# Optimization experiments

Measured on AMD Instinct MI355X. Metric: run time of the kernel, lower is better.

The kernel has to match this reference:

```python
import jax, jax.numpy as jnp
import numpy as np

B, LQ, LK, D = 16, 2048, 2048, 64
EPS = 1e-13
KEEP_PROB = 0.8  # fraction of key positions kept in the mask


def setup_inputs() -> dict:
    key = jax.random.key(0)
    kq, kk, kv, km = jax.random.split(key, 4)
    q = jax.random.normal(kq, (B, LQ, D), dtype=jnp.float32)
    k = jax.random.normal(kk, (B, LK, D), dtype=jnp.float32)
    v = jax.random.normal(kv, (B, LK, D), dtype=jnp.float32)
    # binary 0/1 float mask over key positions (ESIM-style padding mask)
    v_mask = (jax.random.uniform(km, (B, LK)) < KEEP_PROB).astype(jnp.float32)
    return {"q": q, "k": k, "v": v, "v_mask": v_mask}


def masked_softmax(scores, mask):
    # ESIM masked_softmax: softmax(scores * mask) * mask, renormalized.
    m = mask[:, None, :]  # [B, 1, Lk] broadcast over query dim
    p = jax.nn.softmax(scores * m, axis=-1) * m
    return p / (jnp.sum(p, axis=-1, keepdims=True) + EPS)


def reference(q, k, v, v_mask):
    scores = jnp.einsum("bqd,bkd->bqk", q, k)  # [B, Lq, Lk]
    attend = masked_softmax(scores, v_mask)
    return jnp.einsum("bqk,bkd->bqd", attend, v)  # [B, Lq, D]
```

## Files before the change

### kernel.cpp

```cpp
#include <hip/hip_runtime.h>
#include <hip/hip_bf16.h>
#include <stdint.h>

#define NB 16
#define SLQ 2048
#define SLK 2048
#define DD 64
#define BQ 64
#define BK 64
#define NT (SLK / BK)
#define QTILES (SLQ / BQ)
#define LOG2E 1.44269504f

typedef _Float16 f16x8 __attribute__((ext_vector_type(8)));
typedef short s16x8 __attribute__((ext_vector_type(8)));
typedef unsigned int u32x4 __attribute__((ext_vector_type(4)));
typedef unsigned short u16x4 __attribute__((ext_vector_type(4)));
typedef float f32x4 __attribute__((ext_vector_type(4)));
typedef float f32x2 __attribute__((ext_vector_type(2)));

typedef __attribute__((address_space(1))) const void gvoid;
typedef __attribute__((address_space(3))) void lvoid;

__device__ __forceinline__ int swzb(int row, int bytecol) {
    return row * 128 + (bytecol ^ ((row & 7) << 4));
}

__device__ __forceinline__ void gload16(const void* g, void* l) {
    __builtin_amdgcn_global_load_lds((gvoid*)g, (lvoid*)l, 16, 0, 0);
}

__device__ __forceinline__ uint16_t f2bf(float f) {
    __bf16 h = (__bf16)f;
    return __builtin_bit_cast(uint16_t, h);
}
__device__ __forceinline__ float bf2f(uint16_t u) {
    uint32_t x = ((uint32_t)u) << 16;
    return __builtin_bit_cast(float, x);
}

__device__ __forceinline__ int pi64(int x) {
    return (x & 0x23) | ((x & 4) << 2) | ((x >> 1) & 0x0C);
}

__global__ __launch_bounds__(256)
void prep_all(const float* __restrict__ q, const float* __restrict__ k,
              const float* __restrict__ v, const float* __restrict__ vm,
              char* __restrict__ qs, char* __restrict__ ks,
              char* __restrict__ vts, uint16_t* __restrict__ mb16) {
    const int bid = blockIdx.x;
    if (bid < 1024) {
        const int tl = bid & 511;
        const bool isq = bid < 512;
        const float sc = isq ? LOG2E : 1.0f;
        const float* src = (isq ? q : k) + (size_t)tl * (BK * DD);
        char* dst = (isq ? qs : ks) + (size_t)tl * (BK * DD * 2);
        #pragma unroll
        for (int it = 0; it < 2; ++it) {
            int c = threadIdx.x + it * 256;
            int row = c >> 3, col8 = c & 7;
            f32x4 a  = *(const f32x4*)(src + row * DD + col8 * 8);
            f32x4 b2 = *(const f32x4*)(src + row * DD + col8 * 8 + 4);
            f16x8 h;
            #pragma unroll
            for (int j = 0; j < 4; ++j) {
                h[j] = (_Float16)(a[j] * sc);
                h[4 + j] = (_Float16)(b2[j] * sc);
            }
            *(f16x8*)(dst + swzb(row, col8 * 16)) = h;
        }
    } else if (bid < 1536) {
        const int tl = bid - 1024;
        const float* src = v + (size_t)tl * (BK * DD);
        const float* msk = vm + (size_t)tl * BK;
        char* dst = vts + (size_t)tl * (BK * DD * 2);
        const int d = threadIdx.x & 63;
        #pragma unroll
        for (int it = 0; it < 2; ++it) {
            int key8 = (threadIdx.x >> 6) + it * 4;
            s16x8 h;
            #pragma unroll
            for (int j = 0; j < 8; ++j) {
                int kp = key8 * 8 + j;
                int sk = pi64(kp);
                float mv = msk[sk];
                h[j] = (short)f2bf((mv != 0.f) ? src[sk * DD + d] : 0.f);
            }
            *(s16x8*)(dst + swzb(d, key8 * 16)) = h;
        }
    } else {
        int i = (bid - 1536) * 1024 + threadIdx.x * 4;
        int srci = (i & ~63) | pi64(i & 63);
        f32x4 m = *(const f32x4*)(vm + srci);
        u16x4 o;
        #pragma unroll
        for (int j = 0; j < 4; ++j) o[j] = (m[j] != 0.f) ? (uint16_t)0x3F80 : (uint16_t)0;
        *(u16x4*)(mb16 + i) = o;
    }
}

__global__ __launch_bounds__(256, 4)
void attn_fwd(const char* __restrict__ qs, const char* __restrict__ ks,
              const char* __restrict__ vts, const uint16_t* __restrict__ mb16,
              uint16_t* __restrict__ po, float* __restrict__ pl,
              float* __restrict__ out, int nsp)
{
    __shared__ __align__(16) char lk[2][BK * DD * 2];
    __shared__ __align__(16) char lv[2][BK * DD * 2];

    const int tid  = threadIdx.x;
    const int lane = tid & 63;
    const int w    = tid >> 6;
    const int lg   = lane >> 4;
    const int lm   = lane & 15;

    const int G = 512 * nsp;
    int wg = blockIdx.x;
    wg = (wg & 7) * (G >> 3) + (wg >> 3);
    const int qt   = wg & 31;
    const int rest = wg >> 5;
    const int sp   = rest % nsp;
    const int b    = rest / nsp;

    const int qq = NT / nsp, rm = NT % nsp;
    const int t0  = sp * qq + (sp < rm ? sp : rm);
    const int cnt = qq + (sp < rm ? 1 : 0);

    const char* qtile = qs  + (size_t)(b * 32 + qt) * 8192;
    const char* kbase = ks  + (size_t)(b * 32 + t0) * 8192;
    const char* vbase = vts + (size_t)(b * 32 + t0) * 8192;
    const uint16_t* mk = mb16 + (size_t)b * SLK + t0 * BK;

    #pragma unroll
    for (int i = 0; i < 2; ++i) {
        int ch = w * 2 + i;
        gload16(qtile + ch * 1024 + lane * 16, lk[1] + ch * 1024);
    }
    #pragma unroll
    for (int i = 0; i < 2; ++i) {
        int ch = w * 2 + i;
        gload16(kbase + ch * 1024 + lane * 16, lk[0] + ch * 1024);
        gload16(vbase + ch * 1024 + lane * 16, lv[0] + ch * 1024);
    }
    asm volatile("s_waitcnt vmcnt(0)" ::: "memory");
    __syncthreads();

    f16x8 qf[2];
    #pragma unroll
    for (int kc = 0; kc < 2; ++kc)
        qf[kc] = *(const f16x8*)(lk[1] + swzb(w * 16 + lm, kc * 64 + lg * 16));
    asm volatile("s_waitcnt lgkmcnt(0)" ::: "memory");
    __syncthreads();

    f32x4 oacc[4], rsacc;
    #pragma unroll
    for (int d = 0; d < 4; ++d) oacc[d] = (f32x4){0.f, 0.f, 0.f, 0.f};
    rsacc = (f32x4){0.f, 0.f, 0.f, 0.f};

    int buf = 0;
    for (int kt = 0; kt < cnt; ++kt) {
        s16x8 mf0 = *(const s16x8*)(mk + kt * BK + lg * 8);
        s16x8 mf1 = *(const s16x8*)(mk + kt * BK + 32 + lg * 8);

        if (kt + 1 < cnt) {
            const char* kg = kbase + (size_t)(kt + 1) * 8192;
            const char* vg = vbase + (size_t)(kt + 1) * 8192;
            #pragma unroll
            for (int i = 0; i < 2; ++i) {
                int ch = w * 2 + i;
                gload16(kg + ch * 1024 + lane * 16, lk[buf ^ 1] + ch * 1024);
                gload16(vg + ch * 1024 + lane * 16, lv[buf ^ 1] + ch * 1024);
            }
        }

        f32x4 s[4];
        #pragma unroll
        for (int f = 0; f < 4; ++f) s[f] = (f32x4){0.f, 0.f, 0.f, 0.f};
        #pragma unroll
        for (int f = 0; f < 4; ++f) {
            #pragma unroll
            for (int kc = 0; kc < 2; ++kc) {
                f16x8 kf = *(const f16x8*)(lk[buf] + swzb(f * 16 + lm, kc * 64 + lg * 16));
                s[f] = __builtin_amdgcn_mfma_f32_16x16x32_f16(kf, qf[kc], s[f], 0, 0, 0);
            }
        }

        uint32_t pw[8];
        #pragma unroll
        for (int f = 0; f < 4; ++f) {
            float p0 = __builtin_amdgcn_exp2f(s[f][0]);
            float p1 = __builtin_amdgcn_exp2f(s[f][1]);
            float p2 = __builtin_amdgcn_exp2f(s[f][2]);
            float p3 = __builtin_amdgcn_exp2f(s[f][3]);
            pw[f * 2]     = (uint32_t)f2bf(p0) | ((uint32_t)f2bf(p1) << 16);
            pw[f * 2 + 1] = (uint32_t)f2bf(p2) | ((uint32_t)f2bf(p3) << 16);
        }
        u32x4 wa = {pw[0], pw[1], pw[2], pw[3]};
        u32x4 wb = {pw[4], pw[5], pw[6], pw[7]};
        s16x8 pa0 = __builtin_bit_cast(s16x8, wa);
        s16x8 pa1 = __builtin_bit_cast(s16x8, wb);

        rsacc = __builtin_amdgcn_mfma_f32_16x16x32_bf16(pa0, mf0, rsacc, 0, 0, 0);
        rsacc = __builtin_amdgcn_mfma_f32_16x16x32_bf16(pa1, mf1, rsacc, 0, 0, 0);

        #pragma unroll
        for (int d = 0; d < 4; ++d) {
            s16x8 vf0 = *(const s16x8*)(lv[buf] + swzb(d * 16 + lm, lg * 16));
            s16x8 vf1 = *(const s16x8*)(lv[buf] + swzb(d * 16 + lm, 64 + lg * 16));
            oacc[d] = __builtin_amdgcn_mfma_f32_16x16x32_bf16(pa0, vf0, oacc[d], 0, 0, 0);
            oacc[d] = __builtin_amdgcn_mfma_f32_16x16x32_bf16(pa1, vf1, oacc[d], 0, 0, 0);
        }

        asm volatile("s_waitcnt vmcnt(0)" ::: "memory");
        __syncthreads();
        buf ^= 1;
    }

    if (nsp == 1) {
        float* ob = out + ((size_t)b * SLQ + (size_t)qt * BQ) * DD;
        #pragma unroll
        for (int i = 0; i < 4; ++i) {
            float inv = 1.f / (rsacc[i] + 1e-13f);
            int row = w * 16 + lg * 4 + i;
            #pragma unroll
            for (int d = 0; d < 4; ++d)
                ob[row * DD + d * 16 + lm] = oacc[d][i] * inv;
        }
    } else {
        uint16_t* pob = po + (size_t)wg * (BQ * DD);
        #pragma unroll
        for (int i = 0; i < 4; ++i) {
            int row = w * 16 + lg * 4 + i;
            #pragma unroll
            for (int d = 0; d < 4; ++d)
                pob[row * DD + d * 16 + lm] = f2bf(oacc[d][i]);
            if (lm == 0) pl[(size_t)wg * BQ + row] = rsacc[i];
        }
    }
}

__global__ __launch_bounds__(256)
void merge_k(const uint16_t* __restrict__ po, const float* __restrict__ pl,
             float* __restrict__ out, int nsp) {
    const int t  = blockIdx.x;
    const int b  = t >> 5, qt = t & 31;
    const int i0 = (b * nsp) * 32 + qt;
    const int r0 = threadIdx.x >> 4;
    const int c4 = (threadIdx.x & 15) * 4;
    float* ob = out + ((size_t)b * SLQ + (size_t)qt * BQ) * DD;
    #pragma unroll
    for (int rr = 0; rr < BQ; rr += 16) {
        int r = r0 + rr;
        float l = 1e-13f;
        f32x4 acc = (f32x4){0.f, 0.f, 0.f, 0.f};
        for (int s = 0; s < nsp; ++s) {
            int idx = i0 + s * 32;
            l += pl[(size_t)idx * BQ + r];
            u16x4 a = *(const u16x4*)(po + (size_t)idx * (BQ * DD) + r * DD + c4);
            #pragma unroll
            for (int j = 0; j < 4; ++j) acc[j] += bf2f(a[j]);
        }
        float inv = 1.f / l;
        f32x4 o;
        #pragma unroll
        for (int j = 0; j < 4; ++j) o[j] = acc[j] * inv;
        *(f32x4*)(ob + r * DD + c4) = o;
    }
}

__global__ __launch_bounds__(256, 2)
void attn_fallback(const float* __restrict__ q, const float* __restrict__ k,
                   const float* __restrict__ v, const float* __restrict__ vm,
                   float* __restrict__ out)
{
    __shared__ __align__(16) char lqh[64 * DD * 2];
    __shared__ __align__(16) char lql[64 * DD * 2];
    __shared__ __align__(16) char lkh[BK * DD * 2];
    __shared__ __align__(16) char lkl[BK * DD * 2];
    __shared__ __align__(16) char lvt[DD * BK * 2];
    __shared__ __align__(16) char lpp[64 * BK * 2];
    __shared__ float lmask[BK];

    const int tid  = threadIdx.x;
    const int lane = tid & 63;
    const int w    = tid >> 6;
    const int lg   = lane >> 4;
    const int lm   = lane & 15;

    const int b  = blockIdx.y;
    const int qt = blockIdx.x;

    const float* qb = q + ((size_t)b * SLQ + (size_t)qt * 64) * DD;
    const float* kb = k + (size_t)b * SLK * DD;
    const float* vb = v + (size_t)b * SLK * DD;
    const float* mb = vm + (size_t)b * SLK;

    #pragma unroll
    for (int it = 0; it < 2; ++it) {
        int c = tid + it * 256;
        int row = c >> 3, col8 = c & 7;
        f32x4 a  = *(const f32x4*)(qb + row * DD + col8 * 8);
        f32x4 bb = *(const f32x4*)(qb + row * DD + col8 * 8 + 4);
        s16x8 h, l;
        #pragma unroll
        for (int j = 0; j < 4; ++j) {
            uint16_t hh = f2bf(a[j]);
            h[j] = (short)hh; l[j] = (short)f2bf(a[j] - bf2f(hh));
            uint16_t hb = f2bf(bb[j]);
            h[4 + j] = (short)hb; l[4 + j] = (short)f2bf(bb[j] - bf2f(hb));
        }
        *(s16x8*)(lqh + swzb(row, col8 * 16)) = h;
        *(s16x8*)(lql + swzb(row, col8 * 16)) = l;
    }
    __syncthreads();

    s16x8 qfh[2], qfl[2];
    #pragma unroll
    for (int kc = 0; kc < 2; ++kc) {
        qfh[kc] = *(const s16x8*)(lqh + swzb(w * 16 + lm, kc * 64 + lg * 16));
        qfl[kc] = *(const s16x8*)(lql + swzb(w * 16 + lm, kc * 64 + lg * 16));
    }

    float mrow[4], lrow[4];
    f32x4 oacc[4];
    #pragma unroll
    for (int i = 0; i < 4; ++i) { mrow[i] = -1e30f; lrow[i] = 0.f; }
    #pragma unroll
    for (int d = 0; d < 4; ++d) oacc[d] = (f32x4){0.f, 0.f, 0.f, 0.f};

    for (int kt = 0; kt < NT; ++kt) {
        __syncthreads();
        const float* ks2 = kb + (size_t)kt * BK * DD;
        const float* vs = vb + (size_t)kt * BK * DD;

        #pragma unroll
        for (int it = 0; it < 2; ++it) {
            int c = tid + it * 256;
            int row = c >> 3, col8 = c & 7;
            f32x4 a  = *(const f32x4*)(ks2 + row * DD + col8 * 8);
            f32x4 bb = *(const f32x4*)(ks2 + row * DD + col8 * 8 + 4);
            s16x8 h, l;
            #pragma unroll
            for (int j = 0; j < 4; ++j) {
                uint16_t hh = f2bf(a[j]);
                h[j] = (short)hh; l[j] = (short)f2bf(a[j] - bf2f(hh));
                uint16_t hb = f2bf(bb[j]);
                h[4 + j] = (short)hb; l[4 + j] = (short)f2bf(bb[j] - bf2f(hb));
            }
            *(s16x8*)(lkh + swzb(row, col8 * 16)) = h;
            *(s16x8*)(lkl + swzb(row, col8 * 16)) = l;
        }
        #pragma unroll
        for (int it = 0; it < 8; ++it) {
            int c = tid + it * 256;
            int key = c >> 5, dp = (c & 31) * 2;
            f32x2 a = *(const f32x2*)(vs + key * DD + dp);
            *(uint16_t*)(lvt + swzb(dp,     key * 2)) = f2bf(a[0]);
            *(uint16_t*)(lvt + swzb(dp + 1, key * 2)) = f2bf(a[1]);
        }
        if (tid < BK) lmask[tid] = mb[kt * BK + tid];
        __syncthreads();

        f32x4 s[4];
        #pragma unroll
        for (int f = 0; f < 4; ++f) s[f] = (f32x4){0.f, 0.f, 0.f, 0.f};
        #pragma unroll
        for (int f = 0; f < 4; ++f) {
            #pragma unroll
            for (int kc = 0; kc < 2; ++kc) {
                s16x8 kfh = *(const s16x8*)(lkh + swzb(f * 16 + lm, kc * 64 + lg * 16));
                s16x8 kfl = *(const s16x8*)(lkl + swzb(f * 16 + lm, kc * 64 + lg * 16));
                s[f] = __builtin_amdgcn_mfma_f32_16x16x32_bf16(qfh[kc], kfh, s[f], 0, 0, 0);
                s[f] = __builtin_amdgcn_mfma_f32_16x16x32_bf16(qfh[kc], kfl, s[f], 0, 0, 0);
                s[f] = __builtin_amdgcn_mfma_f32_16x16x32_bf16(qfl[kc], kfh, s[f], 0, 0, 0);
            }
        }

        float mv[4];
        #pragma unroll
        for (int f = 0; f < 4; ++f) mv[f] = lmask[f * 16 + lm];

        float pmax[4];
        #pragma unroll
        for (int i = 0; i < 4; ++i) {
            float x = -1e30f;
            #pragma unroll
            for (int f = 0; f < 4; ++f) {
                float sv = (mv[f] != 0.f) ? s[f][i] : -1e30f;
                s[f][i] = sv;
                x = fmaxf(x, sv);
            }
            #pragma unroll
            for (int off = 1; off < 16; off <<= 1)
                x = fmaxf(x, __shfl_xor(x, off, 64));
            pmax[i] = x;
        }

        float scl[4];
        #pragma unroll
        for (int i = 0; i < 4; ++i) {
            float mn = fmaxf(mrow[i], pmax[i]);
            scl[i] = __expf(mrow[i] - mn);
            mrow[i] = mn;
        }
        float rs[4] = {0.f, 0.f, 0.f, 0.f};
        #pragma unroll
        for (int f = 0; f < 4; ++f) {
            #pragma unroll
            for (int i = 0; i < 4; ++i) {
                float p = __expf(s[f][i] - mrow[i]);
                s[f][i] = p;
                rs[i] += p;
            }
        }
        #pragma unroll
        for (int i = 0; i < 4; ++i) {
            #pragma unroll
            for (int off = 1; off < 16; off <<= 1)
                rs[i] += __shfl_xor(rs[i], off, 64);
            lrow[i] = lrow[i] * scl[i] + rs[i];
        }
        #pragma unroll
        for (int d = 0; d < 4; ++d)
            #pragma unroll
            for (int i = 0; i < 4; ++i)
                oacc[d][i] *= scl[i];

        #pragma unroll
        for (int f = 0; f < 4; ++f)
            #pragma unroll
            for (int i = 0; i < 4; ++i)
                *(uint16_t*)(lpp + swzb(w * 16 + lg * 4 + i, (f * 16 + lm) * 2)) = f2bf(s[f][i]);
        __syncthreads();

        #pragma unroll
        for (int kc = 0; kc < 2; ++kc) {
            s16x8 pf = *(const s16x8*)(lpp + swzb(w * 16 + lm, kc * 64 + lg * 16));
            #pragma unroll
            for (int d = 0; d < 4; ++d) {
                s16x8 vf = *(const s16x8*)(lvt + swzb(d * 16 + lm, kc * 64 + lg * 16));
                oacc[d] = __builtin_amdgcn_mfma_f32_16x16x32_bf16(pf, vf, oacc[d], 0, 0, 0);
            }
        }
    }

    float* ob = out + ((size_t)b * SLQ + (size_t)qt * 64) * DD;
    #pragma unroll
    for (int i = 0; i < 4; ++i) {
        float inv = 1.f / (lrow[i] + 1e-13f);
        int row = w * 16 + lg * 4 + i;
        #pragma unroll
        for (int d = 0; d < 4; ++d)
            ob[row * DD + d * 16 + lm] = oacc[d][i] * inv;
    }
}

extern "C" void kernel_launch(void* const* d_in, const int* in_sizes, int n_in,
                              void* d_out, int out_size, void* d_ws, size_t ws_size,
                              hipStream_t stream) {
    const float* q  = (const float*)d_in[0];
    const float* k  = (const float*)d_in[1];
    const float* v  = (const float*)d_in[2];
    const float* vm = (const float*)d_in[3];
    float* out = (float*)d_out;

    const size_t TB     = (size_t)NB * SLK * DD * 2;
    const size_t MB     = (size_t)NB * SLK * 2;
    const size_t PL_PER = (size_t)NB * QTILES * BQ * 4;
    const size_t PO_PER = (size_t)NB * QTILES * BQ * DD * 2;
    const size_t base = 3 * TB + MB;

    int nsp = 0;
    for (int c = 2; c >= 1; --c) {
        if (ws_size >= base + (size_t)c * (PL_PER + PO_PER)) { nsp = c; break; }
    }
    if (nsp == 0) {
        if (ws_size >= base) nsp = 1;
        else {
            dim3 grid(SLQ / 64, NB);
            attn_fallback<<<grid, dim3(256), 0, stream>>>(q, k, v, vm, out);
            return;
        }
    }

    char*     qs   = (char*)d_ws;
    char*     ks   = qs + TB;
    char*     vts  = ks + TB;
    uint16_t* mb16 = (uint16_t*)(vts + TB);
    float*    pl   = (float*)((char*)mb16 + MB);
    uint16_t* po   = (uint16_t*)((char*)pl + (size_t)nsp * PL_PER);

    prep_all<<<dim3(1568), dim3(256), 0, stream>>>(q, k, v, vm, qs, ks, vts, mb16);
    attn_fwd<<<dim3(512 * nsp), dim3(256), 0, stream>>>(qs, ks, vts, mb16, po, pl, out, nsp);
    if (nsp > 1)
        merge_k<<<dim3(NB * QTILES), dim3(256), 0, stream>>>(po, pl, out, nsp);
}
```

Measured before the change: 50.22 us.

## Load V and Q fragments directly from global, drop V LDS buffer, raise occupancy

V tiles are no longer staged through shared memory: each wave reads its V MFMA operands straight from the pre-swizzled global layout, and Q fragments are likewise loaded directly. Halving LDS use allows launch bounds of 6 blocks per CU, and the host now tries a 3-way key split. A partial vmcnt wait lets the V loads complete before the PV MFMAs while the next K tile is still in flight. The cost is more redundant global or L2 traffic for V across waves, higher latency exposure, and more split partials to reduce.

```diff
diff --git a/kernel.cpp b/kernel.cpp
--- a/kernel.cpp
+++ b/kernel.cpp
@@ -99,14 +99,13 @@
     }
 }
 
-__global__ __launch_bounds__(256, 4)
+__global__ __launch_bounds__(256, 6)
 void attn_fwd(const char* __restrict__ qs, const char* __restrict__ ks,
               const char* __restrict__ vts, const uint16_t* __restrict__ mb16,
               uint16_t* __restrict__ po, float* __restrict__ pl,
               float* __restrict__ out, int nsp)
 {
     __shared__ __align__(16) char lk[2][BK * DD * 2];
-    __shared__ __align__(16) char lv[2][BK * DD * 2];
 
     const int tid  = threadIdx.x;
     const int lane = tid & 63;
@@ -131,27 +130,17 @@
     const char* vbase = vts + (size_t)(b * 32 + t0) * 8192;
     const uint16_t* mk = mb16 + (size_t)b * SLK + t0 * BK;
 
-    #pragma unroll
-    for (int i = 0; i < 2; ++i) {
-        int ch = w * 2 + i;
-        gload16(qtile + ch * 1024 + lane * 16, lk[1] + ch * 1024);
-    }
+    f16x8 qf[2];
+    qf[0] = *(const f16x8*)(qtile + swzb(w * 16 + lm, lg * 16));
+    qf[1] = *(const f16x8*)(qtile + swzb(w * 16 + lm, 64 + lg * 16));
     #pragma unroll
     for (int i = 0; i < 2; ++i) {
         int ch = w * 2 + i;
         gload16(kbase + ch * 1024 + lane * 16, lk[0] + ch * 1024);
-        gload16(vbase + ch * 1024 + lane * 16, lv[0] + ch * 1024);
     }
     asm volatile("s_waitcnt vmcnt(0)" ::: "memory");
     __syncthreads();
 
-    f16x8 qf[2];
-    #pragma unroll
-    for (int kc = 0; kc < 2; ++kc)
-        qf[kc] = *(const f16x8*)(lk[1] + swzb(w * 16 + lm, kc * 64 + lg * 16));
-    asm volatile("s_waitcnt lgkmcnt(0)" ::: "memory");
-    __syncthreads();
-
     f32x4 oacc[4], rsacc;
     #pragma unroll
     for (int d = 0; d < 4; ++d) oacc[d] = (f32x4){0.f, 0.f, 0.f, 0.f};
@@ -159,19 +148,29 @@
 
     int buf = 0;
     for (int kt = 0; kt < cnt; ++kt) {
+        const char* vtile = vbase + (size_t)kt * 8192;
+
         s16x8 mf0 = *(const s16x8*)(mk + kt * BK + lg * 8);
         s16x8 mf1 = *(const s16x8*)(mk + kt * BK + 32 + lg * 8);
 
+        s16x8 vf0[4];
+        #pragma unroll
+        for (int d = 0; d < 4; ++d)
+            vf0[d] = *(const s16x8*)(vtile + swzb(d * 16 + lm, lg * 16));
+
         if (kt + 1 < cnt) {
             const char* kg = kbase + (size_t)(kt + 1) * 8192;
-            const char* vg = vbase + (size_t)(kt + 1) * 8192;
             #pragma unroll
             for (int i = 0; i < 2; ++i) {
                 int ch = w * 2 + i;
                 gload16(kg + ch * 1024 + lane * 16, lk[buf ^ 1] + ch * 1024);
-                gload16(vg + ch * 1024 + lane * 16, lv[buf ^ 1] + ch * 1024);
-            }
-        }
+            }
+        }
+
+        s16x8 vf1[4];
+        #pragma unroll
+        for (int d = 0; d < 4; ++d)
+            vf1[d] = *(const s16x8*)(vtile + swzb(d * 16 + lm, 64 + lg * 16));
 
         f32x4 s[4];
         #pragma unroll
@@ -200,15 +199,18 @@
         s16x8 pa0 = __builtin_bit_cast(s16x8, wa);
         s16x8 pa1 = __builtin_bit_cast(s16x8, wb);
 
+        if (kt + 1 < cnt) {
+            asm volatile("s_waitcnt vmcnt(2)" ::: "memory");
+        } else {
+            asm volatile("s_waitcnt vmcnt(0)" ::: "memory");
+        }
+
         rsacc = __builtin_amdgcn_mfma_f32_16x16x32_bf16(pa0, mf0, rsacc, 0, 0, 0);
         rsacc = __builtin_amdgcn_mfma_f32_16x16x32_bf16(pa1, mf1, rsacc, 0, 0, 0);
-
         #pragma unroll
         for (int d = 0; d < 4; ++d) {
-            s16x8 vf0 = *(const s16x8*)(lv[buf] + swzb(d * 16 + lm, lg * 16));
-            s16x8 vf1 = *(const s16x8*)(lv[buf] + swzb(d * 16 + lm, 64 + lg * 16));
-            oacc[d] = __builtin_amdgcn_mfma_f32_16x16x32_bf16(pa0, vf0, oacc[d], 0, 0, 0);
-            oacc[d] = __builtin_amdgcn_mfma_f32_16x16x32_bf16(pa1, vf1, oacc[d], 0, 0, 0);
+            oacc[d] = __builtin_amdgcn_mfma_f32_16x16x32_bf16(pa0, vf0[d], oacc[d], 0, 0, 0);
+            oacc[d] = __builtin_amdgcn_mfma_f32_16x16x32_bf16(pa1, vf1[d], oacc[d], 0, 0, 0);
         }
 
         asm volatile("s_waitcnt vmcnt(0)" ::: "memory");
@@ -471,7 +473,7 @@
     const size_t base = 3 * TB + MB;
 
     int nsp = 0;
-    for (int c = 2; c >= 1; --c) {
+    for (int c = 3; c >= 1; --c) {
         if (ws_size >= base + (size_t)c * (PL_PER + PO_PER)) { nsp = c; break; }
     }
     if (nsp == 0) {
```

New measurement: 127.7 us. 154% more time.
